# Kernel tuning notes

Measured on AMD Instinct MI355X. Metric: run time of the kernel, lower is better.

The kernel has to match this reference:

```python
import jax, jax.numpy as jnp
import numpy as np

N_NODES = 100000


def _gcn_conv(x, W, b, src, dst, n):
    """torch_geometric GCNConv: add self-loops, sym-normalize, x@W, scatter-add."""
    x = x @ W                                   # [n, out]
    loop = jnp.arange(n, dtype=src.dtype)
    src_f = jnp.concatenate([src, loop])        # [E+n]
    dst_f = jnp.concatenate([dst, loop])
    deg = jax.ops.segment_sum(jnp.ones_like(dst_f, dtype=x.dtype), dst_f,
                              num_segments=n)   # in-degree incl. self-loop
    dinv = jnp.where(deg > 0, jax.lax.rsqrt(deg), 0.0)
    norm = dinv[src_f] * dinv[dst_f]            # [E+n]
    msg = x[src_f] * norm[:, None]              # [E+n, out]
    out = jax.ops.segment_sum(msg, dst_f, num_segments=n)
    return out + b


def setup_inputs() -> dict:
    key = jax.random.key(0)
    k1, k2, k3, k4 = jax.random.split(key, 4)
    ninp = 64
    E = 1600000
    edge_index = jax.random.randint(k1, (2, E), 0, N_NODES, dtype=jnp.int64)
    emb = jax.random.normal(k2, (N_NODES, ninp), dtype=jnp.float32) * (1.0 / np.sqrt(ninp))
    W1 = jax.random.normal(k3, (ninp, 2 * ninp), dtype=jnp.float32) * (1.0 / np.sqrt(ninp))
    b1 = jnp.zeros((2 * ninp,), dtype=jnp.float32)
    W2 = jax.random.normal(k4, (2 * ninp, ninp), dtype=jnp.float32) * (1.0 / np.sqrt(2 * ninp))
    b2 = jnp.zeros((ninp,), dtype=jnp.float32)
    return {"edge_index": edge_index, "emb": emb, "W1": W1, "b1": b1, "W2": W2, "b2": b2}


def reference(edge_index, emb, W1, b1, W2, b2):
    src, dst = edge_index[0], edge_index[1]
    h = jax.nn.relu(_gcn_conv(emb, W1, b1, src, dst, N_NODES))
    # dropout: eval mode (identity)
    out = _gcn_conv(h, W2, b2, src, dst, N_NODES)
    return out
```

## Files before the change

### kernel.cpp

```cpp
#include <hip/hip_runtime.h>
#include <cstdint>
#include <cstddef>

#define N_NODES_C 100000
#define NF 64
#define BW 512
#define NB 196
#define CHUNK 8192
#define SORT_CAP 9216

static inline size_t align256(size_t x) { return (x + 255) & ~size_t(255); }

typedef __attribute__((ext_vector_type(8))) short bf16x8;
typedef __attribute__((ext_vector_type(4))) float f32x4;

__device__ inline float bf2f(unsigned short u) { return __uint_as_float(((unsigned)u) << 16); }
__device__ inline unsigned short f2bf(float x) {
    unsigned u = __float_as_uint(x);
    return (unsigned short)((u + 0x7fffu + ((u >> 16) & 1u)) >> 16);
}

__global__ __launch_bounds__(1024) void count_hist(const int* __restrict__ dst, int E,
                                                   int* __restrict__ chunk_hist) {
    __shared__ int hist[NB];
    int t = threadIdx.x;
    for (int i = t; i < NB; i += 1024) hist[i] = 0;
    __syncthreads();
    int e0 = blockIdx.x * CHUNK;
    int e1 = min(e0 + CHUNK, E);
    for (int e = e0 + t; e < e1; e += 1024) atomicAdd(&hist[dst[e] >> 9], 1);
    __syncthreads();
    for (int i = t; i < NB; i += 1024) chunk_hist[blockIdx.x * NB + i] = hist[i];
}

__global__ void scan_cols(const int* __restrict__ chunk_hist, int nbin,
                          int* __restrict__ gpart, int* __restrict__ colsum) {
    int b = blockIdx.x;
    int lane = threadIdx.x;
    int base = 0;
    for (int c0 = 0; c0 < nbin; c0 += 64) {
        int c = c0 + lane;
        int v = (c < nbin) ? chunk_hist[c * NB + b] : 0;
        int x = v;
        #pragma unroll
        for (int d = 1; d < 64; d <<= 1) {
            int y = __shfl_up(x, d, 64);
            if (lane >= d) x += y;
        }
        if (c < nbin) gpart[c * NB + b] = base + x - v;
        base += __shfl(x, 63, 64);
    }
    if (lane == 0) colsum[b] = base;
}

__global__ void scan196b(const int* __restrict__ colsum, int* __restrict__ base196,
                         int* __restrict__ row_start, int n,
                         int* __restrict__ zpadA, int* __restrict__ zpadX) {
    int lane = threadIdx.x;
    zpadA[lane] = 0;
    zpadX[lane] = 0;
    int base = 0;
    for (int c = 0; c < NB; c += 64) {
        int idx = c + lane;
        int v = (idx < NB) ? colsum[idx] : 0;
        int x = v;
        #pragma unroll
        for (int d = 1; d < 64; d <<= 1) {
            int y = __shfl_up(x, d, 64);
            if (lane >= d) x += y;
        }
        if (idx < NB) base196[idx] = base + x - v;
        base += __shfl(x, 63, 64);
    }
    if (lane == 0) { base196[NB] = base; row_start[n] = base; }
}

__global__ __launch_bounds__(1024) void bin_kernel2(const int* __restrict__ src,
                                                    const int* __restrict__ dst, int E,
                                                    const int* __restrict__ chunk_hist,
                                                    const int* __restrict__ gpart,
                                                    const int* __restrict__ base196,
                                                    int* __restrict__ packed) {
    __shared__ int hist[NB];
    __shared__ int lbase[NB];
    __shared__ int lcur[NB];
    __shared__ int dbase[NB];
    __shared__ int stage[CHUNK];
    __shared__ unsigned char bid[CHUNK];
    int t = threadIdx.x;
    int ch = blockIdx.x;
    int e0 = ch * CHUNK;
    int e1 = min(e0 + CHUNK, E);
    for (int i = t; i < NB; i += 1024) {
        hist[i] = chunk_hist[ch * NB + i];
        dbase[i] = base196[i] + gpart[ch * NB + i];
    }
    __syncthreads();
    if (t < 64) {
        int base = 0;
        for (int c = 0; c < NB; c += 64) {
            int idx = c + t;
            int v = (idx < NB) ? hist[idx] : 0;
            int x = v;
            #pragma unroll
            for (int d = 1; d < 64; d <<= 1) {
                int y = __shfl_up(x, d, 64);
                if (t >= d) x += y;
            }
            if (idx < NB) { lbase[idx] = base + x - v; lcur[idx] = base + x - v; }
            base += __shfl(x, 63, 64);
        }
    }
    __syncthreads();
    for (int e = e0 + t; e < e1; e += 1024) {
        int d = dst[e];
        int b = d >> 9;
        int p = atomicAdd(&lcur[b], 1);
        stage[p] = (src[e] << 9) | (d & (BW - 1));
        bid[p] = (unsigned char)b;
    }
    __syncthreads();
    int cnt = e1 - e0;
    for (int i = t; i < cnt; i += 1024) {
        int b = bid[i];
        packed[dbase[b] + (i - lbase[b])] = stage[i];
    }
}

__global__ __launch_bounds__(512) void bucket_sort_deg(const int* __restrict__ base196,
                                                       const int* __restrict__ packed,
                                                       int* __restrict__ sorted_src,
                                                       int* __restrict__ row_start,
                                                       float* __restrict__ dinv, int n) {
    __shared__ int hist[BW];
    __shared__ int cur[BW];
    __shared__ int wsum[8];
    __shared__ int sorted[SORT_CAP];
    int b = blockIdx.x;
    int node0 = b * BW;
    int nn = min(BW, n - node0);
    int base = base196[b];
    int end = base196[b + 1];
    int cnt = end - base;
    int t = threadIdx.x;
    hist[t] = 0;
    __syncthreads();
    for (int i = t; i < cnt; i += 512) atomicAdd(&hist[packed[base + i] & (BW - 1)], 1);
    __syncthreads();
    int v = hist[t];
    int lane = t & 63, w = t >> 6;
    int x = v;
    #pragma unroll
    for (int d = 1; d < 64; d <<= 1) {
        int y = __shfl_up(x, d, 64);
        if (lane >= d) x += y;
    }
    if (lane == 63) wsum[w] = x;
    __syncthreads();
    int woff = 0;
    for (int i = 0; i < w; ++i) woff += wsum[i];
    int excl = woff + x - v;
    cur[t] = excl;
    if (t < nn) {
        row_start[node0 + t] = base + excl;
        dinv[node0 + t] = rsqrtf((float)(v + 1));
    }
    __syncthreads();
    for (int i = t; i < cnt; i += 512) {
        int pk = packed[base + i];
        int p = atomicAdd(&cur[pk & (BW - 1)], 1);
        sorted[p] = pk >> 9;
    }
    __syncthreads();
    for (int i = t; i < cnt; i += 512) sorted_src[base + i] = sorted[i];
}

__global__ __launch_bounds__(256) void prep_w(const float* __restrict__ W1,
                                              const float* __restrict__ W2,
                                              unsigned short* __restrict__ W1f,
                                              unsigned short* __restrict__ W2f) {
    int idx = blockIdx.x * 256 + threadIdx.x;
    int lane = (idx >> 3) & 63;
    int j = idx & 7;
    int kk = (lane >> 4) * 8 + j;
    int cb = lane & 15;
    if (idx < 8192) {
        int frag = idx >> 9;
        int ct = frag >> 1, ks = frag & 1;
        W1f[idx] = f2bf(W1[(ks * 32 + kk) * 128 + ct * 16 + cb]);
    } else {
        int i2 = idx - 8192;
        int frag = i2 >> 9;
        int ct = frag >> 2, ks = frag & 3;
        W2f[i2] = f2bf(W2[(ks * 32 + kk) * 64 + ct * 16 + cb]);
    }
}

__global__ __launch_bounds__(256) void scale_emb(const float* __restrict__ emb,
                                                 const float* __restrict__ dinv,
                                                 unsigned short* __restrict__ Xs, int nq) {
    int q = blockIdx.x * 256 + threadIdx.x;
    if (q >= nq) return;
    int node = q >> 4;
    float d = dinv[node];
    float4 v = ((const float4*)emb)[q];
    ushort4 u;
    u.x = f2bf(v.x * d); u.y = f2bf(v.y * d);
    u.z = f2bf(v.z * d); u.w = f2bf(v.w * d);
    *(ushort4*)&Xs[(size_t)q * 4] = u;
}

template<int OUTBF>
__global__ __launch_bounds__(256) void agg_bf16(const unsigned short* __restrict__ Xs,
                                                const float* __restrict__ dinv,
                                                const int* __restrict__ row_start,
                                                const int* __restrict__ sorted_src,
                                                const float* __restrict__ bias,
                                                void* __restrict__ outp, int n) {
    int lane = threadIdx.x & 63;
    int wid = threadIdx.x >> 6;
    int wave = blockIdx.x * (blockDim.x >> 6) + wid;
    int nwaves = gridDim.x * (blockDim.x >> 6);
    int e = lane >> 4;
    int c = lane & 15;
    const int ZOFF = -64;
    for (int i = wave; i < n; i += nwaves) {
        int s0 = row_start[i], s1 = row_start[i + 1];
        float di = dinv[i];
        ushort4 uself = *(const ushort4*)&Xs[(size_t)i * NF + 4 * c];
        float a0 = 0.f, a1 = 0.f, a2 = 0.f, a3 = 0.f;
        float g0 = 0.f, g1 = 0.f, g2 = 0.f, g3 = 0.f;
        for (int j = s0; j < s1; j += 16) {
            int b0 = j + 4 * e;
            int sj0 = b0, sj1 = b0 + 1, sj2 = b0 + 2, sj3 = b0 + 3;
            int i0 = sorted_src[min(sj0, s1 - 1)];
            int i1 = sorted_src[min(sj1, s1 - 1)];
            int i2 = sorted_src[min(sj2, s1 - 1)];
            int i3 = sorted_src[min(sj3, s1 - 1)];
            int o0 = (sj0 < s1) ? (i0 << 6) : ZOFF;
            int o1 = (sj1 < s1) ? (i1 << 6) : ZOFF;
            int o2 = (sj2 < s1) ? (i2 << 6) : ZOFF;
            int o3 = (sj3 < s1) ? (i3 << 6) : ZOFF;
            ushort4 u0 = *(const ushort4*)(Xs + o0 + 4 * c);
            ushort4 u1 = *(const ushort4*)(Xs + o1 + 4 * c);
            ushort4 u2 = *(const ushort4*)(Xs + o2 + 4 * c);
            ushort4 u3 = *(const ushort4*)(Xs + o3 + 4 * c);
            a0 += bf2f(u0.x); a1 += bf2f(u0.y); a2 += bf2f(u0.z); a3 += bf2f(u0.w);
            g0 += bf2f(u1.x); g1 += bf2f(u1.y); g2 += bf2f(u1.z); g3 += bf2f(u1.w);
            a0 += bf2f(u2.x); a1 += bf2f(u2.y); a2 += bf2f(u2.z); a3 += bf2f(u2.w);
            g0 += bf2f(u3.x); g1 += bf2f(u3.y); g2 += bf2f(u3.z); g3 += bf2f(u3.w);
        }
        a0 += g0; a1 += g1; a2 += g2; a3 += g3;
        a0 += __shfl_xor(a0, 16, 64); a1 += __shfl_xor(a1, 16, 64);
        a2 += __shfl_xor(a2, 16, 64); a3 += __shfl_xor(a3, 16, 64);
        a0 += __shfl_xor(a0, 32, 64); a1 += __shfl_xor(a1, 32, 64);
        a2 += __shfl_xor(a2, 32, 64); a3 += __shfl_xor(a3, 32, 64);
        if (e == 0) {
            a0 = di * (a0 + bf2f(uself.x));
            a1 = di * (a1 + bf2f(uself.y));
            a2 = di * (a2 + bf2f(uself.z));
            a3 = di * (a3 + bf2f(uself.w));
            if (bias) {
                float4 bb = *(const float4*)&bias[4 * c];
                a0 += bb.x; a1 += bb.y; a2 += bb.z; a3 += bb.w;
            }
            if constexpr (OUTBF) {
                unsigned short* out = (unsigned short*)outp;
                ushort4 o;
                o.x = f2bf(a0); o.y = f2bf(a1); o.z = f2bf(a2); o.w = f2bf(a3);
                *(ushort4*)&out[(size_t)i * NF + 4 * c] = o;
            } else {
                float* out = (float*)outp;
                float4 o; o.x = a0; o.y = a1; o.z = a2; o.w = a3;
                *(float4*)&out[(size_t)i * NF + 4 * c] = o;
            }
        }
    }
}

__global__ __launch_bounds__(256) void gemm_mfma(const unsigned short* __restrict__ Abf,
                                                 const unsigned short* __restrict__ W1f,
                                                 const float* __restrict__ b1,
                                                 const unsigned short* __restrict__ W2f,
                                                 const float* __restrict__ dinv,
                                                 unsigned short* __restrict__ Tbf, int n) {
    __shared__ unsigned short h_all[4][16 * 136];
    const int t = threadIdx.x;
    const int wid = t >> 6, lane = t & 63;
    const int m = lane & 15, kg = lane >> 4;
    const int wrow = blockIdx.x * 64 + wid * 16;
    unsigned short* h_lds = h_all[wid];

    int arow = wrow + m; if (arow >= n) arow = n - 1;
    bf16x8 a0 = *(const bf16x8*)&Abf[(size_t)arow * 64 + kg * 8];
    bf16x8 a1 = *(const bf16x8*)&Abf[(size_t)arow * 64 + 32 + kg * 8];

    #pragma unroll
    for (int ct = 0; ct < 8; ++ct) {
        f32x4 acc = {0.f, 0.f, 0.f, 0.f};
        bf16x8 w0 = *(const bf16x8*)&W1f[(ct * 2 + 0) * 512 + lane * 8];
        bf16x8 w1 = *(const bf16x8*)&W1f[(ct * 2 + 1) * 512 + lane * 8];
        acc = __builtin_amdgcn_mfma_f32_16x16x32_bf16(a0, w0, acc, 0, 0, 0);
        acc = __builtin_amdgcn_mfma_f32_16x16x32_bf16(a1, w1, acc, 0, 0, 0);
        float bb = b1[ct * 16 + m];
        #pragma unroll
        for (int r = 0; r < 4; ++r) {
            float v = fmaxf(acc[r] + bb, 0.f);
            h_lds[(kg * 4 + r) * 136 + ct * 16 + m] = f2bf(v);
        }
    }

    bf16x8 hf[4];
    #pragma unroll
    for (int ks = 0; ks < 4; ++ks)
        hf[ks] = *(const bf16x8*)&h_lds[m * 136 + ks * 32 + kg * 8];

    float dv[4];
    #pragma unroll
    for (int r = 0; r < 4; ++r) {
        int row = wrow + kg * 4 + r;
        dv[r] = (row < n) ? dinv[row] : 0.f;
    }
    #pragma unroll
    for (int ct = 0; ct < 4; ++ct) {
        f32x4 acc = {0.f, 0.f, 0.f, 0.f};
        #pragma unroll
        for (int ks = 0; ks < 4; ++ks) {
            bf16x8 w = *(const bf16x8*)&W2f[(ct * 4 + ks) * 512 + lane * 8];
            acc = __builtin_amdgcn_mfma_f32_16x16x32_bf16(hf[ks], w, acc, 0, 0, 0);
        }
        #pragma unroll
        for (int r = 0; r < 4; ++r) {
            int row = wrow + kg * 4 + r;
            if (row < n) Tbf[(size_t)row * 64 + ct * 16 + m] = f2bf(acc[r] * dv[r]);
        }
    }
}

extern "C" void kernel_launch(void* const* d_in, const int* in_sizes, int n_in,
                              void* d_out, int out_size, void* d_ws, size_t ws_size,
                              hipStream_t stream) {
    const int* edge = (const int*)d_in[0];
    const float* emb = (const float*)d_in[1];
    const float* W1  = (const float*)d_in[2];
    const float* b1  = (const float*)d_in[3];
    const float* W2  = (const float*)d_in[4];
    const float* b2  = (const float*)d_in[5];
    int E = in_sizes[0] / 2;
    const int* src = edge;
    const int* dst = edge + E;
    int n = N_NODES_C;
    int nbin = (E + CHUNK - 1) / CHUNK;

    char* p = (char*)d_ws;
    int*   row_start  = (int*)p;   p += align256((size_t)(n + 1) * 4);
    float* dinv       = (float*)p; p += align256((size_t)n * 4);
    int*   base196    = (int*)p;   p += align256(256 * 4);
    int*   colsum     = (int*)p;   p += align256(256 * 4);
    int*   chunk_hist = (int*)p;   p += align256((size_t)nbin * NB * 4);
    int*   gpart      = (int*)p;   p += align256((size_t)nbin * NB * 4);
    unsigned short* W1f = (unsigned short*)p; p += align256(8192 * 2);
    unsigned short* W2f = (unsigned short*)p; p += align256(8192 * 2);
    int*   sorted_src = (int*)p;   p += align256((size_t)E * 4);
    int*   zpadA      = (int*)p;   p += 256;
    unsigned short* Abf = (unsigned short*)p; p += align256((size_t)n * NF * 2);
    int*   zpadX      = (int*)p;   p += 256;
    unsigned short* Xs  = (unsigned short*)p; p += align256((size_t)n * NF * 2);
    int* packed = (int*)Abf;

    prep_w<<<64, 256, 0, stream>>>(W1, W2, W1f, W2f);
    count_hist<<<nbin, 1024, 0, stream>>>(dst, E, chunk_hist);
    scan_cols<<<NB, 64, 0, stream>>>(chunk_hist, nbin, gpart, colsum);
    scan196b<<<1, 64, 0, stream>>>(colsum, base196, row_start, n, zpadA, zpadX);
    bin_kernel2<<<nbin, 1024, 0, stream>>>(src, dst, E, chunk_hist, gpart, base196, packed);
    bucket_sort_deg<<<NB, 512, 0, stream>>>(base196, packed, sorted_src, row_start, dinv, n);

    int nq = n * 16;
    scale_emb<<<(nq + 255) / 256, 256, 0, stream>>>(emb, dinv, Xs, nq);
    agg_bf16<1><<<4096, 256, 0, stream>>>(Xs, dinv, row_start, sorted_src, nullptr, Abf, n);
    gemm_mfma<<<(n + 63) / 64, 256, 0, stream>>>(Abf, W1f, b1, W2f, dinv, Xs, n);
    agg_bf16<0><<<4096, 256, 0, stream>>>(Xs, dinv, row_start, sorted_src, b2, d_out, n);
}
```

Before: 140.6 us.

## Fuse prep kernels into histogram, scan and bucket-sort kernels to cut launches

Weight bf16 prep moves into count_hist, and the 196-bin scan moves into scan_cols using a last-block-done atomic counter. The embedding scaling is fused into bucket_sort_deg, which now runs with 1024 threads and reuses dinv from shared memory. This removes three kernel launches and their serialization gaps. In exchange it adds a threadfence/atomic pattern and a counter reset that relies on count_hist running before scan_cols.

```diff
diff --git a/kernel.cpp b/kernel.cpp
--- a/kernel.cpp
+++ b/kernel.cpp
@@ -21,9 +21,32 @@
 }
 
 __global__ __launch_bounds__(1024) void count_hist(const int* __restrict__ dst, int E,
-                                                   int* __restrict__ chunk_hist) {
+                                                   int* __restrict__ chunk_hist,
+                                                   const float* __restrict__ W1,
+                                                   const float* __restrict__ W2,
+                                                   unsigned short* __restrict__ W1f,
+                                                   unsigned short* __restrict__ W2f,
+                                                   int* __restrict__ done_ctr) {
     __shared__ int hist[NB];
     int t = threadIdx.x;
+    if (blockIdx.x == 0 && t == 0) *done_ctr = 0;
+    int idx = blockIdx.x * 1024 + t;
+    if (idx < 16384) {
+        int lane = (idx >> 3) & 63;
+        int j = idx & 7;
+        int kk = (lane >> 4) * 8 + j;
+        int cb = lane & 15;
+        if (idx < 8192) {
+            int frag = idx >> 9;
+            int ct = frag >> 1, ks = frag & 1;
+            W1f[idx] = f2bf(W1[(ks * 32 + kk) * 128 + ct * 16 + cb]);
+        } else {
+            int i2 = idx - 8192;
+            int frag = i2 >> 9;
+            int ct = frag >> 2, ks = frag & 3;
+            W2f[i2] = f2bf(W2[(ks * 32 + kk) * 64 + ct * 16 + cb]);
+        }
+    }
     for (int i = t; i < NB; i += 1024) hist[i] = 0;
     __syncthreads();
     int e0 = blockIdx.x * CHUNK;
@@ -34,7 +57,10 @@
 }
 
 __global__ void scan_cols(const int* __restrict__ chunk_hist, int nbin,
-                          int* __restrict__ gpart, int* __restrict__ colsum) {
+                          int* __restrict__ gpart, int* __restrict__ colsum,
+                          int* __restrict__ base196, int* __restrict__ row_start, int n,
+                          int* __restrict__ zpadA, int* __restrict__ zpadX,
+                          int* __restrict__ done_ctr) {
     int b = blockIdx.x;
     int lane = threadIdx.x;
     int base = 0;
@@ -51,28 +77,29 @@
         base += __shfl(x, 63, 64);
     }
     if (lane == 0) colsum[b] = base;
-}
-
-__global__ void scan196b(const int* __restrict__ colsum, int* __restrict__ base196,
-                         int* __restrict__ row_start, int n,
-                         int* __restrict__ zpadA, int* __restrict__ zpadX) {
-    int lane = threadIdx.x;
-    zpadA[lane] = 0;
-    zpadX[lane] = 0;
-    int base = 0;
-    for (int c = 0; c < NB; c += 64) {
-        int idx = c + lane;
-        int v = (idx < NB) ? colsum[idx] : 0;
-        int x = v;
-        #pragma unroll
-        for (int d = 1; d < 64; d <<= 1) {
-            int y = __shfl_up(x, d, 64);
-            if (lane >= d) x += y;
-        }
-        if (idx < NB) base196[idx] = base + x - v;
-        base += __shfl(x, 63, 64);
-    }
-    if (lane == 0) { base196[NB] = base; row_start[n] = base; }
+    __threadfence();
+    __shared__ int amlast;
+    if (lane == 0) amlast = (atomicAdd(done_ctr, 1) == NB - 1) ? 1 : 0;
+    __syncthreads();
+    if (amlast) {
+        zpadA[lane] = 0;
+        zpadX[lane] = 0;
+        volatile const int* vcs = colsum;
+        int bb = 0;
+        for (int c = 0; c < NB; c += 64) {
+            int idx2 = c + lane;
+            int v = (idx2 < NB) ? vcs[idx2] : 0;
+            int x = v;
+            #pragma unroll
+            for (int d = 1; d < 64; d <<= 1) {
+                int y = __shfl_up(x, d, 64);
+                if (lane >= d) x += y;
+            }
+            if (idx2 < NB) base196[idx2] = bb + x - v;
+            bb += __shfl(x, 63, 64);
+        }
+        if (lane == 0) { base196[NB] = bb; row_start[n] = bb; }
+    }
 }
 
 __global__ __launch_bounds__(1024) void bin_kernel2(const int* __restrict__ src,
@@ -127,13 +154,16 @@
     }
 }
 
-__global__ __launch_bounds__(512) void bucket_sort_deg(const int* __restrict__ base196,
-                                                       const int* __restrict__ packed,
-                                                       int* __restrict__ sorted_src,
-                                                       int* __restrict__ row_start,
-                                                       float* __restrict__ dinv, int n) {
+__global__ __launch_bounds__(1024) void bucket_sort_deg(const int* __restrict__ base196,
+                                                        const int* __restrict__ packed,
+                                                        int* __restrict__ sorted_src,
+                                                        int* __restrict__ row_start,
+                                                        float* __restrict__ dinv,
+                                                        const float* __restrict__ emb,
+                                                        unsigned short* __restrict__ Xs, int n) {
     __shared__ int hist[BW];
     __shared__ int cur[BW];
+    __shared__ float dloc[BW];
     __shared__ int wsum[8];
     __shared__ int sorted[SORT_CAP];
     int b = blockIdx.x;
@@ -143,71 +173,53 @@
     int end = base196[b + 1];
     int cnt = end - base;
     int t = threadIdx.x;
-    hist[t] = 0;
-    __syncthreads();
-    for (int i = t; i < cnt; i += 512) atomicAdd(&hist[packed[base + i] & (BW - 1)], 1);
-    __syncthreads();
-    int v = hist[t];
     int lane = t & 63, w = t >> 6;
-    int x = v;
-    #pragma unroll
-    for (int d = 1; d < 64; d <<= 1) {
-        int y = __shfl_up(x, d, 64);
-        if (lane >= d) x += y;
-    }
-    if (lane == 63) wsum[w] = x;
-    __syncthreads();
-    int woff = 0;
-    for (int i = 0; i < w; ++i) woff += wsum[i];
-    int excl = woff + x - v;
-    cur[t] = excl;
-    if (t < nn) {
-        row_start[node0 + t] = base + excl;
-        dinv[node0 + t] = rsqrtf((float)(v + 1));
-    }
-    __syncthreads();
-    for (int i = t; i < cnt; i += 512) {
+    if (t < BW) hist[t] = 0;
+    __syncthreads();
+    for (int i = t; i < cnt; i += 1024) atomicAdd(&hist[packed[base + i] & (BW - 1)], 1);
+    __syncthreads();
+    int v = 0, x = 0;
+    if (t < BW) {
+        v = hist[t];
+        x = v;
+        #pragma unroll
+        for (int d = 1; d < 64; d <<= 1) {
+            int y = __shfl_up(x, d, 64);
+            if (lane >= d) x += y;
+        }
+        if (lane == 63) wsum[w] = x;
+    }
+    __syncthreads();
+    if (t < BW) {
+        int woff = 0;
+        for (int i = 0; i < w; ++i) woff += wsum[i];
+        int excl = woff + x - v;
+        cur[t] = excl;
+        float dv_ = rsqrtf((float)(v + 1));
+        dloc[t] = dv_;
+        if (t < nn) {
+            row_start[node0 + t] = base + excl;
+            dinv[node0 + t] = dv_;
+        }
+    }
+    __syncthreads();
+    for (int i = t; i < cnt; i += 1024) {
         int pk = packed[base + i];
         int p = atomicAdd(&cur[pk & (BW - 1)], 1);
         sorted[p] = pk >> 9;
     }
     __syncthreads();
-    for (int i = t; i < cnt; i += 512) sorted_src[base + i] = sorted[i];
-}
-
-__global__ __launch_bounds__(256) void prep_w(const float* __restrict__ W1,
-                                              const float* __restrict__ W2,
-                                              unsigned short* __restrict__ W1f,
-                                              unsigned short* __restrict__ W2f) {
-    int idx = blockIdx.x * 256 + threadIdx.x;
-    int lane = (idx >> 3) & 63;
-    int j = idx & 7;
-    int kk = (lane >> 4) * 8 + j;
-    int cb = lane & 15;
-    if (idx < 8192) {
-        int frag = idx >> 9;
-        int ct = frag >> 1, ks = frag & 1;
-        W1f[idx] = f2bf(W1[(ks * 32 + kk) * 128 + ct * 16 + cb]);
-    } else {
-        int i2 = idx - 8192;
-        int frag = i2 >> 9;
-        int ct = frag >> 2, ks = frag & 3;
-        W2f[i2] = f2bf(W2[(ks * 32 + kk) * 64 + ct * 16 + cb]);
-    }
-}
-
-__global__ __launch_bounds__(256) void scale_emb(const float* __restrict__ emb,
-                                                 const float* __restrict__ dinv,
-                                                 unsigned short* __restrict__ Xs, int nq) {
-    int q = blockIdx.x * 256 + threadIdx.x;
-    if (q >= nq) return;
-    int node = q >> 4;
-    float d = dinv[node];
-    float4 v = ((const float4*)emb)[q];
-    ushort4 u;
-    u.x = f2bf(v.x * d); u.y = f2bf(v.y * d);
-    u.z = f2bf(v.z * d); u.w = f2bf(v.w * d);
-    *(ushort4*)&Xs[(size_t)q * 4] = u;
+    for (int i = t; i < cnt; i += 1024) sorted_src[base + i] = sorted[i];
+    int nq = nn * 16;
+    for (int q = t; q < nq; q += 1024) {
+        int node = node0 + (q >> 4);
+        float d = dloc[q >> 4];
+        float4 vv = *(const float4*)&emb[(size_t)node * 64 + (q & 15) * 4];
+        ushort4 u;
+        u.x = f2bf(vv.x * d); u.y = f2bf(vv.y * d);
+        u.z = f2bf(vv.z * d); u.w = f2bf(vv.w * d);
+        *(ushort4*)&Xs[(size_t)node * 64 + (q & 15) * 4] = u;
+    }
 }
 
 template<int OUTBF>
@@ -357,6 +369,7 @@
     float* dinv       = (float*)p; p += align256((size_t)n * 4);
     int*   base196    = (int*)p;   p += align256(256 * 4);
     int*   colsum     = (int*)p;   p += align256(256 * 4);
+    int*   done_ctr   = (int*)p;   p += align256(4);
     int*   chunk_hist = (int*)p;   p += align256((size_t)nbin * NB * 4);
     int*   gpart      = (int*)p;   p += align256((size_t)nbin * NB * 4);
     unsigned short* W1f = (unsigned short*)p; p += align256(8192 * 2);
@@ -368,15 +381,12 @@
     unsigned short* Xs  = (unsigned short*)p; p += align256((size_t)n * NF * 2);
     int* packed = (int*)Abf;
 
-    prep_w<<<64, 256, 0, stream>>>(W1, W2, W1f, W2f);
-    count_hist<<<nbin, 1024, 0, stream>>>(dst, E, chunk_hist);
-    scan_cols<<<NB, 64, 0, stream>>>(chunk_hist, nbin, gpart, colsum);
-    scan196b<<<1, 64, 0, stream>>>(colsum, base196, row_start, n, zpadA, zpadX);
+    count_hist<<<nbin, 1024, 0, stream>>>(dst, E, chunk_hist, W1, W2, W1f, W2f, done_ctr);
+    scan_cols<<<NB, 64, 0, stream>>>(chunk_hist, nbin, gpart, colsum,
+                                     base196, row_start, n, zpadA, zpadX, done_ctr);
     bin_kernel2<<<nbin, 1024, 0, stream>>>(src, dst, E, chunk_hist, gpart, base196, packed);
-    bucket_sort_deg<<<NB, 512, 0, stream>>>(base196, packed, sorted_src, row_start, dinv, n);
-
-    int nq = n * 16;
-    scale_emb<<<(nq + 255) / 256, 256, 0, stream>>>(emb, dinv, Xs, nq);
+    bucket_sort_deg<<<NB, 1024, 0, stream>>>(base196, packed, sorted_src, row_start, dinv,
+                                             emb, Xs, n);
     agg_bf16<1><<<4096, 256, 0, stream>>>(Xs, dinv, row_start, sorted_src, nullptr, Abf, n);
     gemm_mfma<<<(n + 63) / 64, 256, 0, stream>>>(Abf, W1f, b1, W2f, dinv, Xs, n);
     agg_bf16<0><<<4096, 256, 0, stream>>>(Xs, dinv, row_start, sorted_src, b2, d_out, n);
```

Measured after the change: 137.6 us (median of 2 runs). 2.1% less time.
